# Kernel tuning notes

Hardware: AMD Instinct MI355X
Metric: run time of the kernel (lower is better)

Reference implementation:

```python
import jax, jax.numpy as jnp
import numpy as np

B, L, D = 2, 2048, 1024
H, Z = 16, 64  # n_heads, head_dim


def setup_inputs() -> dict:
    key = jax.random.key(0)
    k1, k2, k3 = jax.random.split(key, 3)
    scale = 1.0 / np.sqrt(D)  # keep projections O(1) for numeric sanity
    x = jax.random.normal(k1, (B, L, D), dtype=jnp.float32)
    Wq = jax.random.normal(k2, (H, Z, D), dtype=jnp.float32) * scale
    Wk = jax.random.normal(k3, (H, Z, D), dtype=jnp.float32) * scale
    beta = jnp.ones((1,), dtype=jnp.float32) / jnp.sqrt(jnp.float32(Z))  # default beta = 1/sqrt(head_dim)
    return {"x": x, "Wq": Wq, "Wk": Wk, "beta": beta}


def _energy(x, Wq, Wk, beta):
    # x: (b, l, d); Wq/Wk: (h, z, d); beta: (1,)
    kp = jnp.einsum('bld,hzd->blhz', x, Wk)
    qp = jnp.einsum('bld,hzd->blhz', x, Wq)
    b0 = beta[0]
    # attention[b,h,q,k] = beta * <k_proj[b,q,h], q_proj[b,k,h]>  (faithful to original index order)
    att = b0 * jnp.einsum('bqhz,bkhz->bhqk', kp, qp)
    e = jax.nn.logsumexp(att, axis=-1)          # (b, h, q)
    e = e.sum(axis=-1).sum(axis=-1)             # (b,)
    return (-1.0 / b0) * e


def reference(x, Wq, Wk, beta):
    # value_and_grad: forward returns (energy, d(energy.sum)/dx)
    def esum(xx):
        return _energy(xx, Wq, Wk, beta).sum()
    en = _energy(x, Wq, Wk, beta)               # (b,)
    gx = jax.grad(esum)(x)                      # (b, l, d)
    return en, gx
```

## Files before the change

kernel.cpp:

```cpp
#include <hip/hip_runtime.h>
#include <math.h>

#define L 2048
#define D 1024
#define H 16
#define Z 64
#define HZ 1024

typedef __bf16 bf16x8 __attribute__((ext_vector_type(8)));
typedef float f32x4 __attribute__((ext_vector_type(4)));
typedef float f32x16 __attribute__((ext_vector_type(16)));

#if __has_builtin(__builtin_amdgcn_exp2f)
#define EXP2(x) __builtin_amdgcn_exp2f(x)
#else
#define EXP2(x) exp2f(x)
#endif

__device__ __forceinline__ void async_ld16(const void* g, void* l) {
  __builtin_amdgcn_global_load_lds(
      (const __attribute__((address_space(1))) uint32_t*)(uintptr_t)g,
      (__attribute__((address_space(3))) uint32_t*)(uint32_t)(uintptr_t)l,
      16, 0, 0);
}

template<int NPIECE>
__device__ __forceinline__ void stage_async(const __bf16* __restrict__ g,
                                            int gstride, char* lds, int tid) {
  const int l = tid & 63, w = tid >> 6;
#pragma unroll
  for (int it = 0; it < NPIECE; ++it) {
    const int region = it * 4 + w;
    const int r = ((region >> 1) << 4) + (l & 15);
    const int c = ((region & 1) << 2) + (l >> 4);
    async_ld16(g + (size_t)r * gstride + c * 8, lds + (region << 10));
  }
}

template<int NPIECE, int NW>
__device__ __forceinline__ void stage_asyncN(const __bf16* __restrict__ g,
                                             int gstride, char* lds,
                                             int l, int wl) {
#pragma unroll
  for (int it = 0; it < NPIECE; ++it) {
    const int region = it * NW + wl;
    const int r = ((region >> 1) << 4) + (l & 15);
    const int c = ((region & 1) << 2) + (l >> 4);
    async_ld16(g + (size_t)r * gstride + c * 8, lds + (region << 10));
  }
}

__device__ __forceinline__ bf16x8 rfrag(const char* lds, int row, int cc) {
  const int region = ((row >> 4) << 1) + (cc >> 2);
  const int slot = (row & 15) + ((cc & 3) << 4);
  return *(const bf16x8*)(lds + region * 1024 + slot * 16);
}

__global__ __launch_bounds__(256) void cvt_kernel(const float* __restrict__ s,
                                                  __bf16* __restrict__ d, int n4) {
  int i = blockIdx.x * 256 + threadIdx.x;
  if (i < n4) {
    float4 v = ((const float4*)s)[i];
    union { __bf16 h[4]; uint2 u; } o;
    o.h[0] = (__bf16)v.x; o.h[1] = (__bf16)v.y;
    o.h[2] = (__bf16)v.z; o.h[3] = (__bf16)v.w;
    ((uint2*)d)[i] = o.u;
  }
}

__global__ __launch_bounds__(256) void wt_kernel(
    const float* __restrict__ Wk, const float* __restrict__ Wq,
    __bf16* __restrict__ Wkb, __bf16* __restrict__ Wqb,
    __bf16* __restrict__ Wkt, __bf16* __restrict__ Wqt) {
  const float* W = blockIdx.z ? Wq : Wk;
  __bf16* Wb = blockIdx.z ? Wqb : Wkb;
  __bf16* Wt = blockIdx.z ? Wqt : Wkt;
  __shared__ __bf16 tile[64][65];
  const int r0 = blockIdx.y * 64, c0 = blockIdx.x * 64;
  const int c = threadIdx.x & 63, rb = threadIdx.x >> 6;
#pragma unroll
  for (int i = 0; i < 16; ++i) {
    int r = rb + i * 4;
    __bf16 v = (__bf16)W[(size_t)(r0 + r) * D + c0 + c];
    tile[r][c] = v;
    Wb[(size_t)(r0 + r) * D + c0 + c] = v;
  }
  __syncthreads();
#pragma unroll
  for (int i = 0; i < 16; ++i) {
    int r = rb + i * 4;
    Wt[(size_t)(c0 + r) * HZ + r0 + c] = tile[c][r];
  }
}

__device__ __forceinline__ int lperm(int mg) {
  const int off = mg & 15;
  return (mg & ~15) | (((off >> 2) & 1) << 3) | (((off >> 3) & 1) << 2);
}

__global__ __launch_bounds__(256, 2) void proj_kernel(
    const __bf16* __restrict__ xb, const __bf16* __restrict__ Wkb,
    const __bf16* __restrict__ Wqb, const float* __restrict__ beta_p,
    __bf16* __restrict__ kp, __bf16* __restrict__ qp,
    __bf16* __restrict__ kpt, __bf16* __restrict__ qpt) {
  const __bf16* __restrict__ Wb = blockIdx.z ? Wqb : Wkb;
  __bf16* __restrict__ outn = blockIdx.z ? qp : kp;
  __bf16* __restrict__ outt = blockIdx.z ? qpt : kpt;
  const int n0 = blockIdx.x * 128, m0 = blockIdx.y * 128;
  const int tid = threadIdx.x, l = tid & 63, w = tid >> 6;
  const int l31 = l & 31, hi = l >> 5;
  const int mh = w >> 1, nh = w & 1;
  const float ab = beta_p[0] * 1.44269504f;
  const float ssc = sqrtf(fabsf(ab));
  const float sc = blockIdx.z ? ssc : ((ab < 0.f) ? -ssc : ssc);
  __shared__ __align__(16) char sA[2][16384], sB[2][16384];

  f32x16 acc[2][2];
#pragma unroll
  for (int mi = 0; mi < 2; ++mi)
#pragma unroll
    for (int ni = 0; ni < 2; ++ni)
#pragma unroll
      for (int i = 0; i < 16; ++i) acc[mi][ni][i] = 0.f;

  const __bf16* __restrict__ Abase = xb + (size_t)m0 * D;
  const __bf16* __restrict__ Bbase = Wb + (size_t)n0 * D;
  stage_async<4>(Abase, D, sA[0], tid);
  stage_async<4>(Bbase, D, sB[0], tid);
  __syncthreads();

  for (int k = 0; k < 16; ++k) {
    const int cur = k & 1, nxt = cur ^ 1;
    if (k < 15) {
      stage_async<4>(Abase + (k + 1) * 64, D, sA[nxt], tid);
      stage_async<4>(Bbase + (k + 1) * 64, D, sB[nxt], tid);
    }
#pragma unroll
    for (int ks = 0; ks < 4; ++ks) {
      bf16x8 am[2], bn[2];
#pragma unroll
      for (int mi = 0; mi < 2; ++mi)
        am[mi] = rfrag(sA[cur], mh * 64 + mi * 32 + l31, 2 * ks + hi);
#pragma unroll
      for (int ni = 0; ni < 2; ++ni)
        bn[ni] = rfrag(sB[cur], nh * 64 + ni * 32 + l31, 2 * ks + hi);
#pragma unroll
      for (int mi = 0; mi < 2; ++mi)
#pragma unroll
        for (int ni = 0; ni < 2; ++ni)
          acc[mi][ni] = __builtin_amdgcn_mfma_f32_32x32x16_bf16(
              am[mi], bn[ni], acc[mi][ni], 0, 0, 0);
    }
    __syncthreads();
  }

  const int b = m0 >> 11;
  const int h = (n0 >> 6) + nh;
  const size_t bh = (size_t)b * H + h;
#pragma unroll
  for (int mi = 0; mi < 2; ++mi)
#pragma unroll
    for (int ni = 0; ni < 2; ++ni) {
      const int z = ni * 32 + l31;
#pragma unroll
      for (int rg = 0; rg < 4; ++rg) {
        const int mloc = mh * 64 + mi * 32 + 8 * rg + 4 * hi;
        const int mg = (m0 & (L - 1)) + mloc;
        union { __bf16 hh[4]; uint2 u; } pk;
#pragma unroll
        for (int j = 0; j < 4; ++j) {
          const float v = acc[mi][ni][4 * rg + j];
          pk.hh[j] = (__bf16)v;
          outn[(bh * L + mg + j) * Z + z] = (__bf16)(v * sc);
        }
        *(uint2*)(outt + (bh * Z + z) * L + lperm(mg)) = pk.u;
      }
    }
}

template<int MODE>
__global__ __launch_bounds__(256, 2) void grad_kernel(
    const __bf16* __restrict__ Rg, const __bf16* __restrict__ Sg,
    const __bf16* __restrict__ Tg,
    float* __restrict__ lse, __bf16* __restrict__ Gout) {
  const int bid = blockIdx.x;
  const int slot = bid >> 3;
  const int bh = (bid & 7) * 4 + (slot >> 4);
  const int qt = slot & 15;
  const int tid = threadIdx.x, l = tid & 63, w = tid >> 6;
  const int wq = w & 1, cg = w >> 1;
  const int l31 = l & 31, hi = l >> 5;
  const int q0 = qt * 128 + wq * 64;
  __shared__ __align__(16) char sM[2][2][2][8192];

  bf16x8 bres0[4], bres1[4];
#pragma unroll
  for (int ks = 0; ks < 4; ++ks) {
    bres0[ks] = *(const bf16x8*)(
        Rg + ((size_t)bh * L + q0 + l31) * Z + ks * 16 + hi * 8);
    bres1[ks] = *(const bf16x8*)(
        Rg + ((size_t)bh * L + q0 + 32 + l31) * Z + ks * 16 + hi * 8);
  }

  f32x16 pv00, pv01, pv10, pv11;
#pragma unroll
  for (int i = 0; i < 16; ++i) { pv00[i] = 0.f; pv01[i] = 0.f; pv10[i] = 0.f; pv11[i] = 0.f; }
  float li0 = 0.f, li1 = 0.f;

  const __bf16* __restrict__ Sbase = Sg + ((size_t)bh * L + cg * 1024) * Z;
  const __bf16* __restrict__ Tbase = Tg + (size_t)bh * Z * L + cg * 1024;

  stage_asyncN<4, 2>(Sbase, Z, sM[cg][0][0], l, wq);
  stage_asyncN<4, 2>(Tbase, L, sM[cg][0][1], l, wq);
  asm volatile("s_waitcnt vmcnt(0)" ::: "memory");
  __builtin_amdgcn_s_barrier();

  for (int kt = 0; kt < 16; ++kt) {
    const int cur = kt & 1, nxt = cur ^ 1;
    if (kt < 15) {
      stage_asyncN<4, 2>(Sbase + (size_t)(kt + 1) * 64 * Z, Z, sM[cg][nxt][0], l, wq);
      stage_asyncN<4, 2>(Tbase + (kt + 1) * 64, L, sM[cg][nxt][1], l, wq);
    }
    bf16x8 av[8], bt[8];
#pragma unroll
    for (int ks = 0; ks < 4; ++ks) {
      av[ks]     = rfrag(sM[cg][cur][0], l31,      2 * ks + hi);
      av[4 + ks] = rfrag(sM[cg][cur][0], 32 + l31, 2 * ks + hi);
      bt[2 * ks]     = rfrag(sM[cg][cur][1], l31,      2 * ks + hi);
      bt[2 * ks + 1] = rfrag(sM[cg][cur][1], 32 + l31, 2 * ks + hi);
    }
    uint32_t P0[2][8], P1[2][8];
    {
      f32x16 st0, st1;
#pragma unroll
      for (int i = 0; i < 16; ++i) { st0[i] = 0.f; st1[i] = 0.f; }
      __builtin_amdgcn_s_setprio(1);
#pragma unroll
      for (int ks = 0; ks < 4; ++ks) {
        st0 = __builtin_amdgcn_mfma_f32_32x32x16_bf16(av[ks], bres0[ks], st0, 0, 0, 0);
        st1 = __builtin_amdgcn_mfma_f32_32x32x16_bf16(av[4 + ks], bres0[ks], st1, 0, 0, 0);
      }
      __builtin_amdgcn_s_setprio(0);
      float lsn = 0.f;
#pragma unroll
      for (int i = 0; i < 8; ++i) {
        float e0 = EXP2(st0[2 * i]), e1 = EXP2(st0[2 * i + 1]);
        float e2 = EXP2(st1[2 * i]), e3 = EXP2(st1[2 * i + 1]);
        if (MODE == 0) lsn += (e0 + e1) + (e2 + e3);
        union { __bf16 hh[2]; uint32_t u; } pk;
        pk.hh[0] = (__bf16)e0; pk.hh[1] = (__bf16)e1; P0[0][i] = pk.u;
        pk.hh[0] = (__bf16)e2; pk.hh[1] = (__bf16)e3; P0[1][i] = pk.u;
      }
      if (MODE == 0) li0 += lsn;
    }
    {
      f32x16 st0, st1;
#pragma unroll
      for (int i = 0; i < 16; ++i) { st0[i] = 0.f; st1[i] = 0.f; }
      __builtin_amdgcn_s_setprio(1);
#pragma unroll
      for (int ks = 0; ks < 4; ++ks) {
        st0 = __builtin_amdgcn_mfma_f32_32x32x16_bf16(av[ks], bres1[ks], st0, 0, 0, 0);
        st1 = __builtin_amdgcn_mfma_f32_32x32x16_bf16(av[4 + ks], bres1[ks], st1, 0, 0, 0);
      }
      __builtin_amdgcn_s_setprio(0);
      float lsn = 0.f;
#pragma unroll
      for (int i = 0; i < 8; ++i) {
        float e0 = EXP2(st0[2 * i]), e1 = EXP2(st0[2 * i + 1]);
        float e2 = EXP2(st1[2 * i]), e3 = EXP2(st1[2 * i + 1]);
        if (MODE == 0) lsn += (e0 + e1) + (e2 + e3);
        union { __bf16 hh[2]; uint32_t u; } pk;
        pk.hh[0] = (__bf16)e0; pk.hh[1] = (__bf16)e1; P1[0][i] = pk.u;
        pk.hh[0] = (__bf16)e2; pk.hh[1] = (__bf16)e3; P1[1][i] = pk.u;
      }
      if (MODE == 0) li1 += lsn;
    }
    __builtin_amdgcn_s_setprio(1);
#pragma unroll
    for (int kc = 0; kc < 4; ++kc) {
      union { uint32_t u[4]; bf16x8 v; } a0, a1;
#pragma unroll
      for (int i = 0; i < 4; ++i) {
        a0.u[i] = P0[kc >> 1][4 * (kc & 1) + i];
        a1.u[i] = P1[kc >> 1][4 * (kc & 1) + i];
      }
      pv00 = __builtin_amdgcn_mfma_f32_32x32x16_bf16(a0.v, bt[2 * kc], pv00, 0, 0, 0);
      pv01 = __builtin_amdgcn_mfma_f32_32x32x16_bf16(a0.v, bt[2 * kc + 1], pv01, 0, 0, 0);
      pv10 = __builtin_amdgcn_mfma_f32_32x32x16_bf16(a1.v, bt[2 * kc], pv10, 0, 0, 0);
      pv11 = __builtin_amdgcn_mfma_f32_32x32x16_bf16(a1.v, bt[2 * kc + 1], pv11, 0, 0, 0);
    }
    __builtin_amdgcn_s_setprio(0);
    if (kt < 15) {
      asm volatile("s_waitcnt vmcnt(0)" ::: "memory");
      __builtin_amdgcn_s_barrier();
    }
  }

  __syncthreads();
  float* red = (float*)sM;
  float* liRed = (float*)((char*)sM + 32768);
  if (cg == 1) {
#pragma unroll
    for (int i = 0; i < 16; ++i) {
      red[(wq * 64 +  0 + i) * 64 + l] = pv00[i];
      red[(wq * 64 + 16 + i) * 64 + l] = pv01[i];
      red[(wq * 64 + 32 + i) * 64 + l] = pv10[i];
      red[(wq * 64 + 48 + i) * 64 + l] = pv11[i];
    }
    if (MODE == 0) {
      liRed[wq * 128 + l] = li0;
      liRed[wq * 128 + 64 + l] = li1;
    }
  }
  __syncthreads();
  if (cg == 1) return;
#pragma unroll
  for (int i = 0; i < 16; ++i) {
    pv00[i] += red[(wq * 64 +  0 + i) * 64 + l];
    pv01[i] += red[(wq * 64 + 16 + i) * 64 + l];
    pv10[i] += red[(wq * 64 + 32 + i) * 64 + l];
    pv11[i] += red[(wq * 64 + 48 + i) * 64 + l];
  }
  if (MODE == 0) {
    li0 += liRed[wq * 128 + l];
    li1 += liRed[wq * 128 + 64 + l];
    li0 += __shfl_xor(li0, 32);
    li1 += __shfl_xor(li1, 32);
  }

  const int b = bh >> 4, head = bh & (H - 1);
#pragma unroll
  for (int r = 0; r < 16; ++r) {
    const int qoff = (r & 3) + 8 * (r >> 2) + 4 * hi;
    float s0 = 1.f, s1 = 1.f;
    if (MODE == 0) {
      s0 = 1.f / __int_as_float(
               __builtin_amdgcn_ds_bpermute(4 * qoff, __float_as_int(li0)));
      s1 = 1.f / __int_as_float(
               __builtin_amdgcn_ds_bpermute(4 * qoff, __float_as_int(li1)));
    }
    const size_t orow0 = ((size_t)b * L + q0 + qoff) * HZ + head * Z;
    const size_t orow1 = ((size_t)b * L + q0 + 32 + qoff) * HZ + head * Z;
    Gout[orow0 + l31]      = (__bf16)(-pv00[r] * s0);
    Gout[orow0 + 32 + l31] = (__bf16)(-pv01[r] * s0);
    Gout[orow1 + l31]      = (__bf16)(-pv10[r] * s1);
    Gout[orow1 + 32 + l31] = (__bf16)(-pv11[r] * s1);
  }
  if (MODE == 0 && hi == 0) {
    lse[(size_t)bh * L + q0 + l31] = __logf(li0);
    lse[(size_t)bh * L + q0 + 32 + l31] = __logf(li1);
  }
}

__global__ __launch_bounds__(256) void kscale_kernel(__bf16* __restrict__ kpt,
                                                     const float* __restrict__ lse) {
  int idx = blockIdx.x * 256 + threadIdx.x;
  int row = idx >> 9;
  int pos4 = (idx & 511) << 2;
  int bh = row >> 6;
  int lbase = (pos4 & ~15) + (((pos4 >> 2) & 1) << 3) + (((pos4 >> 3) & 1) << 2);
  float4 ls = *(const float4*)(lse + (size_t)bh * L + lbase);
  __bf16* p = kpt + (size_t)row * L + pos4;
  union { __bf16 hh[4]; uint2 u; } v;
  v.u = *(uint2*)p;
  v.hh[0] = (__bf16)((float)v.hh[0] * __expf(-ls.x));
  v.hh[1] = (__bf16)((float)v.hh[1] * __expf(-ls.y));
  v.hh[2] = (__bf16)((float)v.hh[2] * __expf(-ls.z));
  v.hh[3] = (__bf16)((float)v.hh[3] * __expf(-ls.w));
  *(uint2*)p = v.u;
}

__global__ __launch_bounds__(256) void energy_kernel(
    const float* __restrict__ lse_ws, const float* __restrict__ beta_p,
    float* __restrict__ out) {
  const int b = blockIdx.x;
  const float* p = lse_ws + (size_t)b * H * L;
  float sum = 0.f;
  for (int i = threadIdx.x; i < H * L; i += 256) sum += p[i];
#pragma unroll
  for (int off = 1; off < 64; off <<= 1) sum += __shfl_xor(sum, off, 64);
  __shared__ float wsum[4];
  if ((threadIdx.x & 63) == 0) wsum[threadIdx.x >> 6] = sum;
  __syncthreads();
  if (threadIdx.x == 0)
    out[b] = -(wsum[0] + wsum[1] + wsum[2] + wsum[3]) / beta_p[0];
}

__global__ __launch_bounds__(256, 2) void gx_kernel(
    const __bf16* __restrict__ Gkp, const __bf16* __restrict__ Gqp,
    const __bf16* __restrict__ Wkt, const __bf16* __restrict__ Wqt,
    float* __restrict__ gx) {
  const int bid = blockIdx.x;
  const int xcd = bid & 7;
  const int nt_ = (bid >> 3) & 7;
  const int mg = bid >> 6;
  const int m0 = (xcd * 8 + mg) * 64;
  const int n0 = nt_ * 128;
  const int tid = threadIdx.x, l = tid & 63, w = tid >> 6;
  const int l31 = l & 31, hi = l >> 5;
  const int mh = w >> 1, nh = w & 1;
  __shared__ __align__(16) char sA[3][8192], sB[3][16384];

  f32x16 acc[2];
#pragma unroll
  for (int ni = 0; ni < 2; ++ni)
#pragma unroll
    for (int i = 0; i < 16; ++i) acc[ni][i] = 0.f;

  auto stageK = [&](int kn, char* a, char* b) {
    const __bf16* __restrict__ An = (kn < 16 ? Gkp : Gqp);
    const __bf16* __restrict__ Bn = (kn < 16 ? Wkt : Wqt);
    const int k0 = (kn & 15) * 64;
    stage_async<2>(An + (size_t)m0 * HZ + k0, HZ, a, tid);
    stage_async<4>(Bn + (size_t)n0 * HZ + k0, HZ, b, tid);
  };

  stageK(0, sA[0], sB[0]);
  stageK(1, sA[1], sB[1]);
  asm volatile("s_waitcnt vmcnt(6)" ::: "memory");
  __builtin_amdgcn_s_barrier();

  const char* a0 = sA[0]; const char* a1 = sA[1]; char* a2 = sA[2];
  const char* b0 = sB[0]; const char* b1 = sB[1]; char* b2 = sB[2];

  for (int kk = 0; kk < 32; ++kk) {
    if (kk < 30) stageK(kk + 2, a2, b2);
#pragma unroll
    for (int ks = 0; ks < 4; ++ks) {
      bf16x8 am, bn[2];
      am = rfrag(a0, mh * 32 + l31, 2 * ks + hi);
#pragma unroll
      for (int ni = 0; ni < 2; ++ni)
        bn[ni] = rfrag(b0, nh * 64 + ni * 32 + l31, 2 * ks + hi);
      __builtin_amdgcn_s_setprio(1);
#pragma unroll
      for (int ni = 0; ni < 2; ++ni)
        acc[ni] = __builtin_amdgcn_mfma_f32_32x32x16_bf16(
            am, bn[ni], acc[ni], 0, 0, 0);
      __builtin_amdgcn_s_setprio(0);
    }
    if (kk < 30) {
      asm volatile("s_waitcnt vmcnt(6)" ::: "memory");
      __builtin_amdgcn_s_barrier();
    } else if (kk == 30) {
      asm volatile("s_waitcnt vmcnt(0)" ::: "memory");
      __builtin_amdgcn_s_barrier();
    }
    const char* x;
    x = a0; a0 = a1; a1 = a2; a2 = (char*)x;
    x = b0; b0 = b1; b1 = b2; b2 = (char*)x;
  }
#pragma unroll
  for (int ni = 0; ni < 2; ++ni) {
    const int n = n0 + nh * 64 + ni * 32 + l31;
#pragma unroll
    for (int r = 0; r < 16; ++r) {
      const int m = m0 + mh * 32 + (r & 3) + 8 * (r >> 2) + 4 * hi;
      gx[(size_t)m * D + n] = acc[ni][r];
    }
  }
}

extern "C" void kernel_launch(void* const* d_in, const int* in_sizes, int n_in,
                              void* d_out, int out_size, void* d_ws, size_t ws_size,
                              hipStream_t stream) {
  const float* x    = (const float*)d_in[0];
  const float* Wq   = (const float*)d_in[1];
  const float* Wk   = (const float*)d_in[2];
  const float* beta = (const float*)d_in[3];
  float* out = (float*)d_out;

  char* ws = (char*)d_ws;
  __bf16* xb  = (__bf16*)(ws);
  __bf16* Wkb = (__bf16*)(ws + (8ull  << 20));
  __bf16* Wqb = (__bf16*)(ws + (10ull << 20));
  __bf16* Wkt = (__bf16*)(ws + (12ull << 20));
  __bf16* Wqt = (__bf16*)(ws + (14ull << 20));
  __bf16* kp  = (__bf16*)(ws + (16ull << 20));
  __bf16* qp  = (__bf16*)(ws + (24ull << 20));
  __bf16* kpt = (__bf16*)(ws + (32ull << 20));
  __bf16* qpt = (__bf16*)(ws + (40ull << 20));
  __bf16* Gkp = (__bf16*)(ws + (48ull << 20));
  __bf16* Gqp = (__bf16*)(ws + (56ull << 20));
  float*  lse = (float*)(ws + (64ull << 20));

  cvt_kernel<<<4096, 256, 0, stream>>>(x, xb, 1048576);
  wt_kernel<<<dim3(16, 16, 2), 256, 0, stream>>>(Wk, Wq, Wkb, Wqb, Wkt, Wqt);
  proj_kernel<<<dim3(8, 32, 2), 256, 0, stream>>>(xb, Wkb, Wqb, beta, kp, qp, kpt, qpt);
  grad_kernel<0><<<512, 256, 0, stream>>>(kp, qp, qpt, lse, Gkp);
  kscale_kernel<<<4096, 256, 0, stream>>>(kpt, lse);
  grad_kernel<1><<<512, 256, 0, stream>>>(qp, kp, kpt, lse, Gqp);
  energy_kernel<<<2, 256, 0, stream>>>(lse, beta, out);
  gx_kernel<<<512, 256, 0, stream>>>(Gkp, Gqp, Wkt, Wqt, out + 2);
}
```

Before: 307.2 us.

## Fuse kpt row scaling into grad kernel epilogue and interleave PV MFMAs

Removes the separate kscale kernel by having grad_kernel<0> scale its own 128-row slice of the transposed key projection by 1/sum-exp in its epilogue, using lane permutes to fetch per-row scales. This saves one launch and avoids re-reading the lse buffer and recomputing exponentials. The PV MFMA accumulation is also split per half so each P tile is consumed right after it is computed, which lowers live registers. Launch bounds become explicit waves_per_eu(2,2). A risk is that the in-epilogue read-modify-write of kpt adds global traffic to the grad kernel's tail.

```diff
diff --git a/kernel.cpp b/kernel.cpp
--- a/kernel.cpp
+++ b/kernel.cpp
@@ -179,10 +179,13 @@
 }
 
 template<int MODE>
-__global__ __launch_bounds__(256, 2) void grad_kernel(
+__global__
+__attribute__((amdgpu_flat_work_group_size(256, 256), amdgpu_waves_per_eu(2, 2)))
+void grad_kernel(
     const __bf16* __restrict__ Rg, const __bf16* __restrict__ Sg,
     const __bf16* __restrict__ Tg,
-    float* __restrict__ lse, __bf16* __restrict__ Gout) {
+    float* __restrict__ lse, __bf16* __restrict__ Gout,
+    __bf16* __restrict__ kscale_t) {
   const int bid = blockIdx.x;
   const int slot = bid >> 3;
   const int bh = (bid & 7) * 4 + (slot >> 4);
@@ -229,7 +232,6 @@
       bt[2 * ks]     = rfrag(sM[cg][cur][1], l31,      2 * ks + hi);
       bt[2 * ks + 1] = rfrag(sM[cg][cur][1], 32 + l31, 2 * ks + hi);
     }
-    uint32_t P0[2][8], P1[2][8];
     {
       f32x16 st0, st1;
 #pragma unroll
@@ -241,6 +243,7 @@
         st1 = __builtin_amdgcn_mfma_f32_32x32x16_bf16(av[4 + ks], bres0[ks], st1, 0, 0, 0);
       }
       __builtin_amdgcn_s_setprio(0);
+      uint32_t P[2][8];
       float lsn = 0.f;
 #pragma unroll
       for (int i = 0; i < 8; ++i) {
@@ -248,10 +251,20 @@
         float e2 = EXP2(st1[2 * i]), e3 = EXP2(st1[2 * i + 1]);
         if (MODE == 0) lsn += (e0 + e1) + (e2 + e3);
         union { __bf16 hh[2]; uint32_t u; } pk;
-        pk.hh[0] = (__bf16)e0; pk.hh[1] = (__bf16)e1; P0[0][i] = pk.u;
-        pk.hh[0] = (__bf16)e2; pk.hh[1] = (__bf16)e3; P0[1][i] = pk.u;
+        pk.hh[0] = (__bf16)e0; pk.hh[1] = (__bf16)e1; P[0][i] = pk.u;
+        pk.hh[0] = (__bf16)e2; pk.hh[1] = (__bf16)e3; P[1][i] = pk.u;
       }
       if (MODE == 0) li0 += lsn;
+      __builtin_amdgcn_s_setprio(1);
+#pragma unroll
+      for (int kc = 0; kc < 4; ++kc) {
+        union { uint32_t u[4]; bf16x8 v; } a;
+#pragma unroll
+        for (int i = 0; i < 4; ++i) a.u[i] = P[kc >> 1][4 * (kc & 1) + i];
+        pv00 = __builtin_amdgcn_mfma_f32_32x32x16_bf16(a.v, bt[2 * kc], pv00, 0, 0, 0);
+        pv01 = __builtin_amdgcn_mfma_f32_32x32x16_bf16(a.v, bt[2 * kc + 1], pv01, 0, 0, 0);
+      }
+      __builtin_amdgcn_s_setprio(0);
     }
     {
       f32x16 st0, st1;
@@ -264,6 +277,7 @@
         st1 = __builtin_amdgcn_mfma_f32_32x32x16_bf16(av[4 + ks], bres1[ks], st1, 0, 0, 0);
       }
       __builtin_amdgcn_s_setprio(0);
+      uint32_t P[2][8];
       float lsn = 0.f;
 #pragma unroll
       for (int i = 0; i < 8; ++i) {
@@ -271,26 +285,21 @@
         float e2 = EXP2(st1[2 * i]), e3 = EXP2(st1[2 * i + 1]);
         if (MODE == 0) lsn += (e0 + e1) + (e2 + e3);
         union { __bf16 hh[2]; uint32_t u; } pk;
-        pk.hh[0] = (__bf16)e0; pk.hh[1] = (__bf16)e1; P1[0][i] = pk.u;
-        pk.hh[0] = (__bf16)e2; pk.hh[1] = (__bf16)e3; P1[1][i] = pk.u;
+        pk.hh[0] = (__bf16)e0; pk.hh[1] = (__bf16)e1; P[0][i] = pk.u;
+        pk.hh[0] = (__bf16)e2; pk.hh[1] = (__bf16)e3; P[1][i] = pk.u;
       }
       if (MODE == 0) li1 += lsn;
-    }
-    __builtin_amdgcn_s_setprio(1);
-#pragma unroll
-    for (int kc = 0; kc < 4; ++kc) {
-      union { uint32_t u[4]; bf16x8 v; } a0, a1;
-#pragma unroll
-      for (int i = 0; i < 4; ++i) {
-        a0.u[i] = P0[kc >> 1][4 * (kc & 1) + i];
-        a1.u[i] = P1[kc >> 1][4 * (kc & 1) + i];
-      }
-      pv00 = __builtin_amdgcn_mfma_f32_32x32x16_bf16(a0.v, bt[2 * kc], pv00, 0, 0, 0);
-      pv01 = __builtin_amdgcn_mfma_f32_32x32x16_bf16(a0.v, bt[2 * kc + 1], pv01, 0, 0, 0);
-      pv10 = __builtin_amdgcn_mfma_f32_32x32x16_bf16(a1.v, bt[2 * kc], pv10, 0, 0, 0);
-      pv11 = __builtin_amdgcn_mfma_f32_32x32x16_bf16(a1.v, bt[2 * kc + 1], pv11, 0, 0, 0);
-    }
-    __builtin_amdgcn_s_setprio(0);
+      __builtin_amdgcn_s_setprio(1);
+#pragma unroll
+      for (int kc = 0; kc < 4; ++kc) {
+        union { uint32_t u[4]; bf16x8 v; } a;
+#pragma unroll
+        for (int i = 0; i < 4; ++i) a.u[i] = P[kc >> 1][4 * (kc & 1) + i];
+        pv10 = __builtin_amdgcn_mfma_f32_32x32x16_bf16(a.v, bt[2 * kc], pv10, 0, 0, 0);
+        pv11 = __builtin_amdgcn_mfma_f32_32x32x16_bf16(a.v, bt[2 * kc + 1], pv11, 0, 0, 0);
+      }
+      __builtin_amdgcn_s_setprio(0);
+    }
     if (kt < 15) {
       asm volatile("s_waitcnt vmcnt(0)" ::: "memory");
       __builtin_amdgcn_s_barrier();
@@ -347,28 +356,42 @@
     Gout[orow1 + l31]      = (__bf16)(-pv10[r] * s1);
     Gout[orow1 + 32 + l31] = (__bf16)(-pv11[r] * s1);
   }
-  if (MODE == 0 && hi == 0) {
-    lse[(size_t)bh * L + q0 + l31] = __logf(li0);
-    lse[(size_t)bh * L + q0 + 32 + l31] = __logf(li1);
-  }
-}
-
-__global__ __launch_bounds__(256) void kscale_kernel(__bf16* __restrict__ kpt,
-                                                     const float* __restrict__ lse) {
-  int idx = blockIdx.x * 256 + threadIdx.x;
-  int row = idx >> 9;
-  int pos4 = (idx & 511) << 2;
-  int bh = row >> 6;
-  int lbase = (pos4 & ~15) + (((pos4 >> 2) & 1) << 3) + (((pos4 >> 3) & 1) << 2);
-  float4 ls = *(const float4*)(lse + (size_t)bh * L + lbase);
-  __bf16* p = kpt + (size_t)row * L + pos4;
-  union { __bf16 hh[4]; uint2 u; } v;
-  v.u = *(uint2*)p;
-  v.hh[0] = (__bf16)((float)v.hh[0] * __expf(-ls.x));
-  v.hh[1] = (__bf16)((float)v.hh[1] * __expf(-ls.y));
-  v.hh[2] = (__bf16)((float)v.hh[2] * __expf(-ls.z));
-  v.hh[3] = (__bf16)((float)v.hh[3] * __expf(-ls.w));
-  *(uint2*)p = v.u;
+  if (MODE == 0) {
+    if (hi == 0) {
+      lse[(size_t)bh * L + q0 + l31] = __logf(li0);
+      lse[(size_t)bh * L + q0 + 32 + l31] = __logf(li1);
+    }
+    const float rli0 = 1.f / li0, rli1 = 1.f / li1;
+    const int pos4 = (l & 7) * 4;
+    const int lb = lperm(pos4);
+    float sf0[4], sf1[4];
+#pragma unroll
+    for (int j = 0; j < 4; ++j) {
+      sf0[j] = __int_as_float(
+          __builtin_amdgcn_ds_bpermute(4 * (lb + j), __float_as_int(rli0)));
+      sf1[j] = __int_as_float(
+          __builtin_amdgcn_ds_bpermute(4 * (lb + j), __float_as_int(rli1)));
+    }
+    __bf16* krow = kscale_t + ((size_t)bh * Z + (l >> 3)) * L + q0 + pos4;
+#pragma unroll
+    for (int pass = 0; pass < 8; ++pass) {
+      union { __bf16 hh[4]; uint2 u; } v;
+      v.u = *(uint2*)krow;
+      v.hh[0] = (__bf16)((float)v.hh[0] * sf0[0]);
+      v.hh[1] = (__bf16)((float)v.hh[1] * sf0[1]);
+      v.hh[2] = (__bf16)((float)v.hh[2] * sf0[2]);
+      v.hh[3] = (__bf16)((float)v.hh[3] * sf0[3]);
+      *(uint2*)krow = v.u;
+      union { __bf16 hh[4]; uint2 u; } v2;
+      v2.u = *(uint2*)(krow + 32);
+      v2.hh[0] = (__bf16)((float)v2.hh[0] * sf1[0]);
+      v2.hh[1] = (__bf16)((float)v2.hh[1] * sf1[1]);
+      v2.hh[2] = (__bf16)((float)v2.hh[2] * sf1[2]);
+      v2.hh[3] = (__bf16)((float)v2.hh[3] * sf1[3]);
+      *(uint2*)(krow + 32) = v2.u;
+      krow += (size_t)8 * L;
+    }
+  }
 }
 
 __global__ __launch_bounds__(256) void energy_kernel(
@@ -488,9 +511,8 @@
   cvt_kernel<<<4096, 256, 0, stream>>>(x, xb, 1048576);
   wt_kernel<<<dim3(16, 16, 2), 256, 0, stream>>>(Wk, Wq, Wkb, Wqb, Wkt, Wqt);
   proj_kernel<<<dim3(8, 32, 2), 256, 0, stream>>>(xb, Wkb, Wqb, beta, kp, qp, kpt, qpt);
-  grad_kernel<0><<<512, 256, 0, stream>>>(kp, qp, qpt, lse, Gkp);
-  kscale_kernel<<<4096, 256, 0, stream>>>(kpt, lse);
-  grad_kernel<1><<<512, 256, 0, stream>>>(qp, kp, kpt, lse, Gqp);
+  grad_kernel<0><<<512, 256, 0, stream>>>(kp, qp, qpt, lse, Gkp, kpt);
+  grad_kernel<1><<<512, 256, 0, stream>>>(qp, kp, kpt, lse, Gqp, kpt);
   energy_kernel<<<2, 256, 0, stream>>>(lse, beta, out);
   gx_kernel<<<512, 256, 0, stream>>>(Gkp, Gqp, Wkt, Wqt, out + 2);
 }
```

Measured after the change: 311.6 us. Within noise of the previous version (+1.4%).
